# Performance work log

Measured on AMD Instinct MI355X. Metric: run time of the kernel, lower is better.

Reference implementation:

```python
import jax, jax.numpy as jnp
import numpy as np

SEQ, B, H = 4096, 128, 128


def setup_inputs() -> dict:
    key = jax.random.key(0)
    ks = jax.random.split(key, 5)
    s = 1.0 / np.sqrt(H)
    return {
        "sequence": jax.random.normal(ks[0], (SEQ, B, H), dtype=jnp.float32),
        "init_state": jnp.zeros((2, 1, H), dtype=jnp.float32),
        "W_in0": jax.random.normal(ks[1], (H, H), dtype=jnp.float32) * s,
        "W_h0": jax.random.normal(ks[2], (H, H), dtype=jnp.float32) * s,
        "W_in1": jax.random.normal(ks[3], (H, H), dtype=jnp.float32) * s,
        "W_h1": jax.random.normal(ks[4], (H, H), dtype=jnp.float32) * s,
    }


def _run_layer(seq, h0, W_in, W_h):
    # h_{t} = gelu(h_{t-1} @ W_h^T + x_t @ W_in^T)  (torch Linear: x @ W.T, bias=False)
    # Precompute input projection for all timesteps in one big GEMM (same math).
    xin = jnp.einsum('sbi,hi->sbh', seq, W_in)

    def step(h, x):
        h = jax.nn.gelu(h @ W_h.T + x, approximate=False)
        return h, h

    h_final, states = jax.lax.scan(step, h0, xin)
    return states, h_final


def reference(sequence, init_state, W_in0, W_h0, W_in1, W_h1):
    batch = sequence.shape[1]
    hid = init_state.shape[2]
    finals = []
    # NOTE: faithful to source — every layer consumes the ORIGINAL sequence,
    # and only the last layer's states are returned.
    h0 = jnp.broadcast_to(init_state[0], (batch, hid))
    states, h = _run_layer(sequence, h0, W_in0, W_h0)
    finals.append(h)
    h0 = jnp.broadcast_to(init_state[1], (batch, hid))
    states, h = _run_layer(sequence, h0, W_in1, W_h1)
    finals.append(h)
    # torch.cat of (batch, hidden) tensors along dim 0 -> (num_layers*batch, hidden)
    final_hiddens = jnp.concatenate(finals, axis=0)
    return states, final_hiddens
```

## Files before the change

### kernel.cpp

```cpp
#include <hip/hip_runtime.h>
#include <math.h>

#define SEQ 4096
#define B   128
#define H   128
#define TPB 512
#define BH  (B * H)

typedef float v2f __attribute__((ext_vector_type(2)));
typedef float v4f __attribute__((ext_vector_type(4)));

template <int CTRL>
__device__ __forceinline__ float dpp_movf(float v) {
    int i = __builtin_bit_cast(int, v);
    int r = __builtin_amdgcn_update_dpp(0, i, CTRL, 0xF, 0xF, false);
    return __builtin_bit_cast(float, r);
}
#define DPP_XOR1 0xB1
#define DPP_XOR2 0x4E
#define DPP_ROR8 0x128
#define DPP_ROR4 0x124

__global__ __launch_bounds__(TPB, 2) void rnn_persist(
    const float* __restrict__ seq,
    const float* __restrict__ init,
    const float* __restrict__ Win0, const float* __restrict__ Wh0,
    const float* __restrict__ Win1, const float* __restrict__ Wh1,
    float* __restrict__ out)
{
    __shared__ float h_lds[2][H];

    const int tid = threadIdx.x;
    const int bid = blockIdx.x;
    const int l   = bid >> 7;
    const int b   = bid & (B - 1);
    const int ks  = tid & 15;
    const int jg  = tid >> 4;
    const int o1  = (ks >> 1) & 1, o0 = ks & 1;

    const float* Win = l ? Win1 : Win0;
    const float* Wh  = l ? Wh1  : Wh0;

    v2f win[4][4], wh[4][4];
#pragma unroll
    for (int i = 0; i < 4; ++i) {
        const int b1 = (i >> 1) & 1, c = i & 1;
        const int jr = jg * 4 + 2 * (b1 ^ o1) + (c ^ o0);
        const float* wi = Win + jr * H + ks * 8;
        const float* wp = Wh  + jr * H + ks * 8;
#pragma unroll
        for (int q = 0; q < 4; ++q) {
            win[i][q] = *(const v2f*)(wi + 2 * q);
            wh [i][q] = *(const v2f*)(wp + 2 * q);
        }
    }

    if (tid < H) h_lds[0][tid] = init[l * H + tid];

    const float* xbase = seq + (size_t)b * H + 8 * ks;
    v4f xA0 = *(const v4f*)(xbase);
    v4f xA1 = *(const v4f*)(xbase + 4);
    v4f xB0 = *(const v4f*)(xbase + (size_t)BH);
    v4f xB1 = *(const v4f*)(xbase + (size_t)BH + 4);
    v4f xC0 = *(const v4f*)(xbase + 2 * (size_t)BH);
    v4f xC1 = *(const v4f*)(xbase + 2 * (size_t)BH + 4);
    v4f xD0 = *(const v4f*)(xbase + 3 * (size_t)BH);
    v4f xD1 = *(const v4f*)(xbase + 3 * (size_t)BH + 4);

    float* out_states = out + (size_t)b * H;
    const bool l1 = (l == 1);
    const bool wr = (ks < 4);
    const int  jw = jg * 4 + ks;

    __syncthreads();

#define STEP(CUR, NXT, X0, X1, T)                                              \
    do {                                                                       \
        v4f xa = X0, xb = X1;                                                  \
        if ((T) + 4 < SEQ) {     \
            X0 = *(const v4f*)(xbase + (size_t)((T) + 4) * BH);                \
            X1 = *(const v4f*)(xbase + (size_t)((T) + 4) * BH + 4);            \
        }                                                                      \
        v4f ha = *(const v4f*)&h_lds[CUR][8 * ks];                             \
        v4f hb = *(const v4f*)&h_lds[CUR][8 * ks + 4];                         \
        v2f xp0 = {xa.x, xa.y}, xp1 = {xa.z, xa.w};                            \
        v2f xp2 = {xb.x, xb.y}, xp3 = {xb.z, xb.w};                            \
        v2f hp0 = {ha.x, ha.y}, hp1 = {ha.z, ha.w};                            \
        v2f hp2 = {hb.x, hb.y}, hp3 = {hb.z, hb.w};                            \
        float p[4];                                                            \
        _Pragma("unroll")                                                      \
        for (int i = 0; i < 4; ++i) {                                          \
            v2f acc = xp0 * win[i][0];                                         \
            acc += xp1 * win[i][1];                                            \
            acc += xp2 * win[i][2];                                            \
            acc += xp3 * win[i][3];                                            \
            acc += hp0 * wh[i][0];                                             \
            acc += hp1 * wh[i][1];                                             \
            acc += hp2 * wh[i][2];                                             \
            acc += hp3 * wh[i][3];                                             \
            p[i] = acc.x + acc.y;                                              \
        }                                                                      \
               \
        float q0 = p[0] + dpp_movf<DPP_XOR1>(p[1]);                            \
        float q1 = p[2] + dpp_movf<DPP_XOR1>(p[3]);                            \
        float r  = q0 + dpp_movf<DPP_XOR2>(q1);                                \
        float s  = r  + dpp_movf<DPP_ROR8>(r);                                 \
        float S  = s  + dpp_movf<DPP_ROR4>(s);     \
        float g  = 0.5f * S * (1.0f + erff(S * 0.70710678118654752f));         \
        if (wr) {                                                              \
            h_lds[NXT][jw] = g;                                                \
            if (l1) out_states[(size_t)(T) * BH + jw] = g;                     \
        }                                                                      \
        __syncthreads();                                                       \
    } while (0)

    for (int t = 0; t < SEQ; t += 4) {
        STEP(0, 1, xA0, xA1, t);
        STEP(1, 0, xB0, xB1, t + 1);
        STEP(0, 1, xC0, xC1, t + 2);
        STEP(1, 0, xD0, xD1, t + 3);
    }
#undef STEP

    if (tid < H)
        out[(size_t)SEQ * BH + ((size_t)l * B + b) * H + tid] = h_lds[0][tid];
}

extern "C" void kernel_launch(void* const* d_in, const int* in_sizes, int n_in,
                              void* d_out, int out_size, void* d_ws, size_t ws_size,
                              hipStream_t stream) {
    const float* seq  = (const float*)d_in[0];
    const float* init = (const float*)d_in[1];
    const float* Win0 = (const float*)d_in[2];
    const float* Wh0  = (const float*)d_in[3];
    const float* Win1 = (const float*)d_in[4];
    const float* Wh1  = (const float*)d_in[5];
    float* out = (float*)d_out;

    rnn_persist<<<2 * B, TPB, 0, stream>>>(seq, init, Win0, Wh0, Win1, Wh1, out);
}
```

Before: 2.403 ms.

## Use LDS-only barrier, polynomial erf GELU, and swizzled hidden-state LDS layout

Replaces __syncthreads with an inline-asm barrier that waits only on LDS counters, so the in-flight prefetch loads of future x and the output stores no longer have to drain every step. Replaces erff with an Abramowitz-Stegun style polynomial using hardware rcp/exp2, which shortens the serial per-step dependency chain at the cost of lower accuracy. It also pads and swizzles the hidden-state LDS array to reduce bank conflicts, and pins the weight registers with empty asm. The approximate erf risks tolerance failures, and the hand-written barrier depends on the compiler inserting the right waits for the prefetched loads before they are used.

```diff
diff --git a/kernel.cpp b/kernel.cpp
--- a/kernel.cpp
+++ b/kernel.cpp
@@ -21,6 +21,28 @@
 #define DPP_ROR8 0x128
 #define DPP_ROR4 0x124
 
+#define BLOCK_SYNC_NO_VMDRAIN() \
+    asm volatile("s_waitcnt lgkmcnt(0)\n\ts_barrier" ::: "memory")
+
+__device__ __forceinline__ float gelu_erf(float v) {
+    float z  = v * 0.70710678118654752f;
+    float az = __builtin_fabsf(z);
+    float t  = __builtin_amdgcn_rcpf(fmaf(0.3275911f, az, 1.0f));
+    float p  = fmaf(1.061405429f, t, -1.453152027f);
+    p = fmaf(p, t, 1.421413741f);
+    p = fmaf(p, t, -0.284496736f);
+    p = fmaf(p, t, 0.254829592f);
+    p = p * t;
+    float e  = __builtin_amdgcn_exp2f(az * az * -1.4426950408889634f);
+    float er = fmaf(-p, e, 1.0f);
+    er = __builtin_copysignf(er, z);
+    float hv = 0.5f * v;
+    return fmaf(hv, er, hv);
+}
+
+__device__ __forceinline__ int hswz(int j) { return j + (((j >> 5) & 3) << 2); }
+#define HPAD 140
+
 __global__ __launch_bounds__(TPB, 2) void rnn_persist(
     const float* __restrict__ seq,
     const float* __restrict__ init,
@@ -28,7 +50,7 @@
     const float* __restrict__ Win1, const float* __restrict__ Wh1,
     float* __restrict__ out)
 {
-    __shared__ float h_lds[2][H];
+    __shared__ float h_lds[2][HPAD];
 
     const int tid = threadIdx.x;
     const int bid = blockIdx.x;
@@ -54,35 +76,44 @@
             wh [i][q] = *(const v2f*)(wp + 2 * q);
         }
     }
+#pragma unroll
+    for (int i = 0; i < 4; ++i) {
+        asm volatile("" : "+v"(win[i][0]), "+v"(win[i][1]),
+                          "+v"(win[i][2]), "+v"(win[i][3]),
+                          "+v"(wh[i][0]),  "+v"(wh[i][1]),
+                          "+v"(wh[i][2]),  "+v"(wh[i][3]));
+    }
 
-    if (tid < H) h_lds[0][tid] = init[l * H + tid];
+    if (tid < H) h_lds[0][hswz(tid)] = init[l * H + tid];
 
-    const float* xbase = seq + (size_t)b * H + 8 * ks;
-    v4f xA0 = *(const v4f*)(xbase);
-    v4f xA1 = *(const v4f*)(xbase + 4);
-    v4f xB0 = *(const v4f*)(xbase + (size_t)BH);
-    v4f xB1 = *(const v4f*)(xbase + (size_t)BH + 4);
-    v4f xC0 = *(const v4f*)(xbase + 2 * (size_t)BH);
-    v4f xC1 = *(const v4f*)(xbase + 2 * (size_t)BH + 4);
-    v4f xD0 = *(const v4f*)(xbase + 3 * (size_t)BH);
-    v4f xD1 = *(const v4f*)(xbase + 3 * (size_t)BH + 4);
+    const float* xs  = seq + (size_t)b * H;
+    const int    xo  = 8 * ks;
+    v4f xA0 = *(const v4f*)(xs + xo);
+    v4f xA1 = *(const v4f*)(xs + xo + 4);
+    v4f xB0 = *(const v4f*)(xs + (size_t)BH + xo);
+    v4f xB1 = *(const v4f*)(xs + (size_t)BH + xo + 4);
+    v4f xC0 = *(const v4f*)(xs + 2 * (size_t)BH + xo);
+    v4f xC1 = *(const v4f*)(xs + 2 * (size_t)BH + xo + 4);
+    v4f xD0 = *(const v4f*)(xs + 3 * (size_t)BH + xo);
+    v4f xD1 = *(const v4f*)(xs + 3 * (size_t)BH + xo + 4);
 
     float* out_states = out + (size_t)b * H;
     const bool l1 = (l == 1);
     const bool wr = (ks < 4);
     const int  jw = jg * 4 + ks;
+    const int  jws = hswz(jw);
 
     __syncthreads();
 
 #define STEP(CUR, NXT, X0, X1, T)                                              \
     do {                                                                       \
         v4f xa = X0, xb = X1;                                                  \
-        if ((T) + 4 < SEQ) {     \
-            X0 = *(const v4f*)(xbase + (size_t)((T) + 4) * BH);                \
-            X1 = *(const v4f*)(xbase + (size_t)((T) + 4) * BH + 4);            \
+        if ((T) + 4 < SEQ) {                \
+            X0 = *(const v4f*)(xs + (size_t)((T) + 4) * BH + xo);              \
+            X1 = *(const v4f*)(xs + (size_t)((T) + 4) * BH + xo + 4);          \
         }                                                                      \
-        v4f ha = *(const v4f*)&h_lds[CUR][8 * ks];                             \
-        v4f hb = *(const v4f*)&h_lds[CUR][8 * ks + 4];                         \
+        v4f ha = *(const v4f*)&h_lds[CUR][hswz(8 * ks)];                       \
+        v4f hb = *(const v4f*)&h_lds[CUR][hswz(8 * ks + 4)];                   \
         v2f xp0 = {xa.x, xa.y}, xp1 = {xa.z, xa.w};                            \
         v2f xp2 = {xb.x, xb.y}, xp3 = {xb.z, xb.w};                            \
         v2f hp0 = {ha.x, ha.y}, hp1 = {ha.z, ha.w};                            \
@@ -106,12 +137,12 @@
         float r  = q0 + dpp_movf<DPP_XOR2>(q1);                                \
         float s  = r  + dpp_movf<DPP_ROR8>(r);                                 \
         float S  = s  + dpp_movf<DPP_ROR4>(s);     \
-        float g  = 0.5f * S * (1.0f + erff(S * 0.70710678118654752f));         \
+        float g  = gelu_erf(S);                                                \
         if (wr) {                                                              \
-            h_lds[NXT][jw] = g;                                                \
+            h_lds[NXT][jws] = g;                                               \
             if (l1) out_states[(size_t)(T) * BH + jw] = g;                     \
         }                                                                      \
-        __syncthreads();                                                       \
+        BLOCK_SYNC_NO_VMDRAIN();                                               \
     } while (0)
 
     for (int t = 0; t < SEQ; t += 4) {
@@ -123,7 +154,8 @@
 #undef STEP
 
     if (tid < H)
-        out[(size_t)SEQ * BH + ((size_t)l * B + b) * H + tid] = h_lds[0][tid];
+        out[(size_t)SEQ * BH + ((size_t)l * B + b) * H + tid] =
+            h_lds[0][hswz(tid)];
 }
 
 extern "C" void kernel_launch(void* const* d_in, const int* in_sizes, int n_in,
```

Measured after the change: 1.992 ms. -17.1%, faster.
